# Kernel tuning notes

Hardware: AMD Instinct MI355X
Metric: run time of the kernel (lower is better)

## Reference

```python
import jax, jax.numpy as jnp
import numpy as np
import math

DIM_EMB = 1024
DIM_QK = 1024
DIM_V = 1024
NORM_FACT = 1.0 / math.sqrt(DIM_EMB)

def setup_inputs() -> dict:
    key = jax.random.key(0)
    k0, k1, k2, k3 = jax.random.split(key, 4)
    x = jax.random.normal(k0, (4, 4096, DIM_EMB), dtype=jnp.float32)
    # nn.Linear weights are [out_features, in_features]; y = x @ W.T
    s = 1.0 / math.sqrt(DIM_EMB)
    Wq = jax.random.uniform(k1, (DIM_QK, DIM_EMB), jnp.float32, -s, s)
    Wk = jax.random.uniform(k2, (DIM_QK, DIM_EMB), jnp.float32, -s, s)
    Wv = jax.random.uniform(k3, (DIM_V, DIM_EMB), jnp.float32, -s, s)
    return {"x": x, "Wq": Wq, "Wk": Wk, "Wv": Wv}

def reference(x, Wq, Wk, Wv):
    # q,k,v: [b, n, d]
    q = jnp.einsum('bne,de->bnd', x, Wq)
    k = jnp.einsum('bne,de->bnd', x, Wk)
    v = jnp.einsum('bne,de->bnd', x, Wv)
    logits = jnp.einsum('bnd,bmd->bnm', q, k)  # [b, n, n]
    # Faithful to source: softmax over last dim FIRST, then scale by 1/sqrt(dim_embedding)
    score = jax.nn.softmax(logits, axis=-1) * NORM_FACT
    att = jnp.einsum('bnm,bmv->bnv', score, v)
    return att
```

## Files before the change

kernel.cpp:

```cpp
#include <hip/hip_runtime.h>
#include <hip/hip_bf16.h>

typedef _Float16 f16;
typedef _Float16 f16x4 __attribute__((ext_vector_type(4)));
typedef _Float16 f16x8 __attribute__((ext_vector_type(8)));
typedef float f32x4 __attribute__((ext_vector_type(4)));

__device__ __forceinline__ void gload16(const void* g, void* l) {
    __builtin_amdgcn_global_load_lds(
        (const __attribute__((address_space(1))) void*)g,
        (__attribute__((address_space(3))) void*)l, 16, 0, 0);
}

#define FENCE asm volatile("" ::: "memory")
#define BARRIER do { FENCE; __builtin_amdgcn_s_barrier(); FENCE; } while (0)

#define PHASE_MFMA(QI, QJ)                                                    \
    __builtin_amdgcn_s_setprio(1);                                            \
    _Pragma("unroll")                                                         \
    for (int ks = 0; ks < 2; ++ks)                                            \
      _Pragma("unroll")                                                       \
      for (int i = 0; i < 4; ++i)                                             \
        _Pragma("unroll")                                                     \
        for (int j = 0; j < 2; ++j)                                           \
          acc[(QI)*4 + i][(QJ)*2 + j] = __builtin_amdgcn_mfma_f32_16x16x32_f16( \
              a[i][ks], b[j][ks], acc[(QI)*4 + i][(QJ)*2 + j], 0, 0, 0);      \
    __builtin_amdgcn_s_setprio(0);

#define BT8_BODY(KBASE, NTILES)                                               \
    const int rr8 = lane >> 3;                                                \
    const int cs  = ((lane & 7) ^ rr8) << 3;                                  \
    const int ldsr = wid << 3;                                                \
    auto stageA = [&](int kt, int c, int h) {                                 \
        const size_t g0 = (size_t)(bm + (h << 7) + ldsr + rr8) * lda + (KBASE) + kt + cs; \
        gload16(A + g0,                      &sA[c][((h << 7) + ldsr) << 6]); \
        gload16(A + g0 + ((size_t)lda << 6), &sA[c][((h << 7) + 64 + ldsr) << 6]); \
    };                                                                        \
    auto stageB = [&](int kt, int c, int h) {                                 \
        const size_t g0 = (size_t)(bn + (h << 7) + ldsr + rr8) * ldb + (KBASE) + kt + cs; \
        gload16(B + g0,                      &sB[c][((h << 7) + ldsr) << 6]); \
        gload16(B + g0 + ((size_t)ldb << 6), &sB[c][((h << 7) + 64 + ldsr) << 6]); \
    };                                                                        \
    f32x4 acc[8][4] = {};                                                     \
    f16x8 a[4][2], b[2][2];                                                   \
    auto loadA = [&](int c, int qi) {                                         \
        _Pragma("unroll")                                                     \
        for (int i = 0; i < 4; ++i) {                                         \
            const int ra = wr * 128 + (qi * 4 + i) * 16 + (lane & 15);        \
            const int swz = (ra & 7) << 3;                                    \
            _Pragma("unroll")                                                 \
            for (int ks = 0; ks < 2; ++ks) {                                  \
                const int kk = ks * 32 + (lane >> 4) * 8;                     \
                a[i][ks] = *(const f16x8*)(&sA[c][(ra << 6) + (kk ^ swz)]);   \
            }                                                                 \
        }                                                                     \
    };                                                                        \
    auto loadB = [&](int c, int qj) {                                         \
        _Pragma("unroll")                                                     \
        for (int j = 0; j < 2; ++j) {                                         \
            const int rb = wc * 64 + (qj * 2 + j) * 16 + (lane & 15);         \
            const int swz = (rb & 7) << 3;                                    \
            _Pragma("unroll")                                                 \
            for (int ks = 0; ks < 2; ++ks) {                                  \
                const int kk = ks * 32 + (lane >> 4) * 8;                     \
                b[j][ks] = *(const f16x8*)(&sB[c][(rb << 6) + (kk ^ swz)]);   \
            }                                                                 \
        }                                                                     \
    };                                                                        \
    stageA(0, 0, 0); stageA(0, 0, 1); stageB(0, 0, 0); stageB(0, 0, 1);       \
    for (int g = 0; g < (NTILES); ++g) {                                      \
        const int c = g & 1, cn = c ^ 1;                                      \
        const int kn = (g + 1) << 6;                                          \
        const bool more = (g + 1) < (NTILES);                                 \
              \
        if (more) {                                                           \
            stageA(kn, cn, 0); stageA(kn, cn, 1);                             \
            asm volatile("s_waitcnt vmcnt(4)" ::: "memory");                  \
        } else {                                                              \
            asm volatile("s_waitcnt vmcnt(0)" ::: "memory");                  \
        }                                                                     \
        BARRIER;                                                              \
        loadA(c, 0); loadB(c, 0);                                             \
        BARRIER; PHASE_MFMA(0, 0); BARRIER;                                   \
                                       \
        if (more) { stageB(kn, cn, 0); stageB(kn, cn, 1); }                   \
        loadB(c, 1);                                                          \
        BARRIER; PHASE_MFMA(0, 1); BARRIER;                                   \
                                                                     \
        loadA(c, 1); loadB(c, 0);                                             \
        BARRIER; PHASE_MFMA(1, 0); BARRIER;                                   \
                                                                     \
        loadB(c, 1);                                                          \
        BARRIER; PHASE_MFMA(1, 1); BARRIER;                                   \
    }

template<bool F16OUT>
__global__ __launch_bounds__(512) void gemm_bt8(
    const f16* __restrict__ A, const f16* __restrict__ B, void* __restrict__ Cv,
    int K, int lda, int ldb, int ldc, float scale, int nbn)
{
    __shared__ f16 sA[2][256 * 64];
    __shared__ f16 sB[2][256 * 64];
    const int tid = threadIdx.x, lane = tid & 63, wid = tid >> 6;
    const int wr = wid >> 2, wc = wid & 3;
    const int cpx = gridDim.x >> 3;
    const int wg = (blockIdx.x & 7) * cpx + (blockIdx.x >> 3);
    const int bm = (wg / nbn) << 8, bn = (wg % nbn) << 8;

    BT8_BODY(0, K >> 6)

#pragma unroll
    for (int i = 0; i < 8; ++i)
#pragma unroll
        for (int j = 0; j < 4; ++j)
#pragma unroll
            for (int r = 0; r < 4; ++r) {
                const int row = bm + wr * 128 + i * 16 + ((lane >> 4) << 2) + r;
                const int col = bn + wc * 64 + j * 16 + (lane & 15);
                if constexpr (F16OUT)
                    ((f16*)Cv)[(size_t)row * ldc + col] = (f16)(acc[i][j][r] * scale);
                else
                    ((float*)Cv)[(size_t)row * ldc + col] = acc[i][j][r] * scale;
            }
}

__global__ __launch_bounds__(512) void gemm_qk(
    const f16* __restrict__ A, const f16* __restrict__ B,
    f16* __restrict__ S, int lda, int ldb)
{
    __shared__ f16 sA[2][256 * 64];
    __shared__ f16 sB[2][256 * 64];
    const int tid = threadIdx.x, lane = tid & 63, wid = tid >> 6;
    const int wr = wid >> 2, wc = wid & 3;
    const int cpx = gridDim.x >> 3;
    const int wg = (blockIdx.x & 7) * cpx + (blockIdx.x >> 3);
    const int bm = (wg >> 4) << 8, bn = (wg & 15) << 8;

    BT8_BODY(0, 16)

    {
        f16* Tb = wr ? (f16*)sB : (f16*)sA;
        const int lg = lane >> 4;
#pragma unroll
        for (int i = 0; i < 8; ++i)
#pragma unroll
            for (int j = 0; j < 4; ++j)
#pragma unroll
                for (int r = 0; r < 4; ++r) {
                    const int rloc = i * 16 + lg * 4 + r;
                    const int col  = wc * 64 + j * 16 + (lane & 15);
                    Tb[rloc * 256 + (col ^ (((rloc >> 2) & 7) << 3))] = (f16)acc[i][j][r];
                }
    }
    BARRIER;
#pragma unroll
    for (int u = 0; u < 16; ++u) {
        const int gi = u * 512 + tid;
        const int row = gi >> 5;
        const int c0 = (gi & 31) << 3;
        const f16* Tb = (row & 128) ? (const f16*)sB : (const f16*)sA;
        f16x8 v = *(const f16x8*)(Tb + (row & 127) * 256
                                  + (c0 ^ (((row >> 2) & 7) << 3)));
        *(f16x8*)(S + (size_t)(bm + row) * 4096 + bn + c0) = v;
    }
}

__global__ __launch_bounds__(256) void softmax_f16(f16* S)
{
    const int lane = threadIdx.x & 63, wid = threadIdx.x >> 6;
    const int row = blockIdx.x * 4 + wid;
    f16* src = S + (size_t)row * 4096;
    f16x8 v[8];
#pragma unroll
    for (int u = 0; u < 8; ++u) v[u] = *(const f16x8*)(src + u * 512 + lane * 8);
    float m = -1e30f;
#pragma unroll
    for (int u = 0; u < 8; ++u)
#pragma unroll
        for (int e = 0; e < 8; ++e) m = fmaxf(m, (float)v[u][e]);
#pragma unroll
    for (int msk = 1; msk <= 32; msk <<= 1) m = fmaxf(m, __shfl_xor(m, msk));
    float ev[64];
    float s = 0.f;
#pragma unroll
    for (int u = 0; u < 8; ++u)
#pragma unroll
        for (int e = 0; e < 8; ++e) {
            const float x = __expf((float)v[u][e] - m);
            ev[u * 8 + e] = x; s += x;
        }
#pragma unroll
    for (int msk = 1; msk <= 32; msk <<= 1) s += __shfl_xor(s, msk);
    const float inv = 1.0f / (32.0f * s);
#pragma unroll
    for (int u = 0; u < 8; ++u) {
        f16x8 p;
#pragma unroll
        for (int e = 0; e < 8; ++e) p[e] = (f16)(ev[u * 8 + e] * inv);
        *(f16x8*)(src + u * 512 + lane * 8) = p;
    }
}

__global__ __launch_bounds__(512) void gemm_pv8(
    const f16* __restrict__ A, const f16* __restrict__ B, float* __restrict__ Cout,
    f16* __restrict__ Pp, int lda, int ldb)
{
    __shared__ f16 sA[2][256 * 64];
    __shared__ f16 sB[2][256 * 64];
    const int tid = threadIdx.x, lane = tid & 63, wid = tid >> 6;
    const int wr = wid >> 2, wc = wid & 3;
    const int cpx = gridDim.x >> 3;
    const int wg = (blockIdx.x & 7) * cpx + (blockIdx.x >> 3);
    const int bm = (wg >> 2) << 8, bn = (wg & 3) << 8;
    const int z = blockIdx.y;
    const int kbase = z << 10;

    BT8_BODY(kbase, 16)

#pragma unroll
    for (int i = 0; i < 8; ++i)
#pragma unroll
        for (int j = 0; j < 4; ++j)
#pragma unroll
            for (int r = 0; r < 4; ++r) {
                const int row = bm + wr * 128 + i * 16 + ((lane >> 4) << 2) + r;
                const int col = bn + wc * 64 + j * 16 + (lane & 15);
                const float v = acc[i][j][r];
                if (z == 3)
                    Cout[((size_t)row << 10) + col] = v;
                else
                    Pp[(size_t)z * 4194304 + ((size_t)row << 10) + col] = (f16)v;
            }
}

__global__ __launch_bounds__(256) void reduce_pv(
    float* __restrict__ Cout, const f16* __restrict__ Pp)
{
    const int i = blockIdx.x * 256 + threadIdx.x;
    const int r = i >> 7;
    const int c = (i & 127) << 3;
    const size_t base = ((size_t)r << 10) + c;
    const f16x8 p0 = *(const f16x8*)(Pp + base);
    const f16x8 p1 = *(const f16x8*)(Pp + base + 4194304);
    const f16x8 p2 = *(const f16x8*)(Pp + base + 8388608);
    float* o = Cout + base;
    float4 o0 = *(float4*)o, o1 = *(float4*)(o + 4);
    o0.x += (float)p0[0] + (float)p1[0] + (float)p2[0];
    o0.y += (float)p0[1] + (float)p1[1] + (float)p2[1];
    o0.z += (float)p0[2] + (float)p1[2] + (float)p2[2];
    o0.w += (float)p0[3] + (float)p1[3] + (float)p2[3];
    o1.x += (float)p0[4] + (float)p1[4] + (float)p2[4];
    o1.y += (float)p0[5] + (float)p1[5] + (float)p2[5];
    o1.z += (float)p0[6] + (float)p1[6] + (float)p2[6];
    o1.w += (float)p0[7] + (float)p1[7] + (float)p2[7];
    *(float4*)o = o0;
    *(float4*)(o + 4) = o1;
}

__global__ __launch_bounds__(256) void gemm_vt(
    const f16* __restrict__ A, const f16* __restrict__ B, f16* __restrict__ C,
    int K, int lda, int ldb, int ldc)
{
    __shared__ f16 sA[2][128 * 64];
    __shared__ f16 sB[2][128 * 64];
    const int tid = threadIdx.x, lane = tid & 63, wid = tid >> 6;
    const int wr = wid >> 1, wc = wid & 1;
    const int bm = blockIdx.x * 128, bn = blockIdx.y * 128;

    f32x4 acc[4][4] = {};

    auto stage16 = [&](int kt, int bsel) {
        const int rsub = lane >> 3;
        const int csw = ((lane & 7) ^ rsub) << 3;
#pragma unroll
        for (int i = 0; i < 4; ++i) {
            const int rb = (wid * 4 + i) * 8;
            gload16(A + (size_t)(bm + rb + rsub) * lda + kt + csw, &sA[bsel][rb * 64]);
            gload16(B + (size_t)(bn + rb + rsub) * ldb + kt + csw, &sB[bsel][rb * 64]);
        }
    };

    auto compute = [&](int bsel) {
#pragma unroll
        for (int ks = 0; ks < 2; ++ks) {
            const int kk = ks * 32 + (lane >> 4) * 8;
            f16x8 a[4], b[4];
#pragma unroll
            for (int i = 0; i < 4; ++i) {
                const int ra = wr * 64 + i * 16 + (lane & 15);
                a[i] = *(const f16x8*)(&sA[bsel][(ra << 6) + (kk ^ ((ra & 7) << 3))]);
                const int rb2 = wc * 64 + i * 16 + (lane & 15);
                b[i] = *(const f16x8*)(&sB[bsel][(rb2 << 6) + (kk ^ ((rb2 & 7) << 3))]);
            }
#pragma unroll
            for (int i = 0; i < 4; ++i)
#pragma unroll
                for (int j = 0; j < 4; ++j)
                    acc[i][j] = __builtin_amdgcn_mfma_f32_16x16x32_f16(a[i], b[j], acc[i][j], 0, 0, 0);
        }
    };

    stage16(0, 0);
    asm volatile("s_waitcnt vmcnt(0)" ::: "memory");
    __syncthreads();
    const int NT2 = K >> 6;
    for (int t = 0; t < NT2; ++t) {
        if (t + 1 < NT2) stage16((t + 1) << 6, (t + 1) & 1);
        compute(t & 1);
        asm volatile("s_waitcnt vmcnt(0)" ::: "memory");
        __builtin_amdgcn_s_barrier();
    }
#pragma unroll
    for (int i = 0; i < 4; ++i)
#pragma unroll
        for (int j = 0; j < 4; ++j)
#pragma unroll
            for (int r = 0; r < 4; ++r) {
                const int row = bm + wr * 64 + i * 16 + (lane >> 4) * 4 + r;
                const int col = bn + wc * 64 + j * 16 + (lane & 15);
                C[(size_t)row * ldc + col] = (f16)acc[i][j][r];
            }
}

__global__ __launch_bounds__(256) void cvt3(
    const float* __restrict__ x, const float* __restrict__ wq, const float* __restrict__ wk,
    f16* __restrict__ dx, f16* __restrict__ dwq, f16* __restrict__ dwk)
{
    const int i = blockIdx.x * 256 + threadIdx.x;
    const float* s; f16* d; int off;
    if (i < 2097152)      { s = x;  d = dx;  off = i; }
    else if (i < 2228224) { s = wq; d = dwq; off = i - 2097152; }
    else                  { s = wk; d = dwk; off = i - 2228224; }
    const float4 a = ((const float4*)s)[off * 2];
    const float4 b = ((const float4*)s)[off * 2 + 1];
    f16x8 o = { (f16)a.x, (f16)a.y, (f16)a.z, (f16)a.w,
                (f16)b.x, (f16)b.y, (f16)b.z, (f16)b.w };
    ((f16x8*)d)[off] = o;
}

__global__ __launch_bounds__(256) void cvt_batch(
    const float* __restrict__ xb, const float* __restrict__ wv,
    f16* __restrict__ dxb, f16* __restrict__ dwv)
{
    const int i = blockIdx.x * 256 + threadIdx.x;
    const float* s; f16* d; int off;
    if (i < 524288) { s = xb; d = dxb; off = i; }
    else            { s = wv; d = dwv; off = i - 524288; }
    const float4 a = ((const float4*)s)[off * 2];
    const float4 b = ((const float4*)s)[off * 2 + 1];
    f16x8 o = { (f16)a.x, (f16)a.y, (f16)a.z, (f16)a.w,
                (f16)b.x, (f16)b.y, (f16)b.z, (f16)b.w };
    ((f16x8*)d)[off] = o;
}

extern "C" void kernel_launch(void* const* d_in, const int* in_sizes, int n_in,
                              void* d_out, int out_size, void* d_ws, size_t ws_size,
                              hipStream_t stream) {
    const float* x  = (const float*)d_in[0];
    const float* Wq = (const float*)d_in[1];
    const float* Wk = (const float*)d_in[2];
    const float* Wv = (const float*)d_in[3];
    float* out = (float*)d_out;

    f16*   qk  = (f16*)d_out;
    f16*   xh  = (f16*)d_ws;
    f16*   wqh = (f16*)((char*)d_ws + (32LL << 20));
    f16*   wkh = wqh + 1024LL * 1024;

    f16*   S   = (f16*)d_ws;
    f16*   Pp  = (f16*)((char*)d_ws + (32LL << 20));
    f16*   vTw = (f16*)((char*)d_ws + (56LL << 20));

    cvt3<<<9216, 256, 0, stream>>>(x, Wq, Wk, xh, wqh, wkh);

    gemm_bt8<true><<<256, 512, 0, stream>>>(xh, wqh, qk,        1024, 1024, 1024, 2048, 1.f, 4);
    gemm_bt8<true><<<256, 512, 0, stream>>>(xh, wkh, qk + 1024, 1024, 1024, 1024, 2048, 1.f, 4);

    for (int b = 0; b < 4; ++b) {
        const size_t tb = (size_t)b * 4096;
        f16* xhb = (f16*)(out + tb * 1024);
        f16* wvh = xhb + 4096LL * 1024;
        gemm_qk<<<256, 512, 0, stream>>>(
            qk + tb * 2048, qk + tb * 2048 + 1024, S, 2048, 2048);
        softmax_f16<<<1024, 256, 0, stream>>>(S);
        cvt_batch<<<2560, 256, 0, stream>>>(x + tb * 1024, Wv, xhb, wvh);
        gemm_vt<<<dim3(8, 32), 256, 0, stream>>>(wvh, xhb, vTw, 1024, 1024, 1024, 4096);
        gemm_pv8<<<dim3(64, 4), 512, 0, stream>>>(S, vTw, out + tb * 1024, Pp, 4096, 4096);
        reduce_pv<<<2048, 256, 0, stream>>>(out + tb * 1024, Pp);
    }
}
```

Before: 673.5 us.

## Unroll GEMM k-loop by two and spread async LDS stages across MFMA phases

Restructures the shared GEMM main loop into a two-tile unrolled schedule. Global-to-LDS stage loads are interleaved at finer granularity between the MFMA phases, and the B register fragments are kept for both column halves so they no longer need reloading. The number of barriers per tile drops from eight to four. The aim is more overlap of memory traffic with MFMA work and fewer LDS reads. The cost is more registers, and the loop now assumes an even tile count.

```diff
diff --git a/kernel.cpp b/kernel.cpp
--- a/kernel.cpp
+++ b/kernel.cpp
@@ -24,7 +24,7 @@
         _Pragma("unroll")                                                     \
         for (int j = 0; j < 2; ++j)                                           \
           acc[(QI)*4 + i][(QJ)*2 + j] = __builtin_amdgcn_mfma_f32_16x16x32_f16( \
-              a[i][ks], b[j][ks], acc[(QI)*4 + i][(QJ)*2 + j], 0, 0, 0);      \
+              a[i][ks], b[(QJ)*2 + j][ks], acc[(QI)*4 + i][(QJ)*2 + j], 0, 0, 0); \
     __builtin_amdgcn_s_setprio(0);
 
 #define BT8_BODY(KBASE, NTILES)                                               \
@@ -42,7 +42,7 @@
         gload16(B + g0 + ((size_t)ldb << 6), &sB[c][((h << 7) + 64 + ldsr) << 6]); \
     };                                                                        \
     f32x4 acc[8][4] = {};                                                     \
-    f16x8 a[4][2], b[2][2];                                                   \
+    f16x8 a[4][2], b[4][2];                                                   \
     auto loadA = [&](int c, int qi) {                                         \
         _Pragma("unroll")                                                     \
         for (int i = 0; i < 4; ++i) {                                         \
@@ -50,7 +50,7 @@
             const int swz = (ra & 7) << 3;                                    \
             _Pragma("unroll")                                                 \
             for (int ks = 0; ks < 2; ++ks) {                                  \
-                const int kk = ks * 32 + (lane >> 4) * 8;                     \
+                const int kk = ks * 32 + ((lane >> 4) << 3);                  \
                 a[i][ks] = *(const f16x8*)(&sA[c][(ra << 6) + (kk ^ swz)]);   \
             }                                                                 \
         }                                                                     \
@@ -62,36 +62,63 @@
             const int swz = (rb & 7) << 3;                                    \
             _Pragma("unroll")                                                 \
             for (int ks = 0; ks < 2; ++ks) {                                  \
-                const int kk = ks * 32 + (lane >> 4) * 8;                     \
-                b[j][ks] = *(const f16x8*)(&sB[c][(rb << 6) + (kk ^ swz)]);   \
+                const int kk = ks * 32 + ((lane >> 4) << 3);                  \
+                b[qj * 2 + j][ks] = *(const f16x8*)(&sB[c][(rb << 6) + (kk ^ swz)]); \
             }                                                                 \
         }                                                                     \
     };                                                                        \
+            \
     stageA(0, 0, 0); stageA(0, 0, 1); stageB(0, 0, 0); stageB(0, 0, 1);       \
-    for (int g = 0; g < (NTILES); ++g) {                                      \
-        const int c = g & 1, cn = c ^ 1;                                      \
-        const int kn = (g + 1) << 6;                                          \
-        const bool more = (g + 1) < (NTILES);                                 \
-              \
+    stageA(64, 1, 0);                                                         \
+    for (int g2 = 0; g2 < (NTILES); g2 += 2) {                                \
+        const bool more = (g2 + 2) < (NTILES);                                \
+        const int kO  = (g2 + 1) << 6;                                        \
+        const int kE2 = (g2 + 2) << 6;                                        \
+        const int kO2 = (g2 + 3) << 6;                                        \
+           \
+        stageA(kO, 1, 1); stageB(kO, 1, 0);                                   \
+        asm volatile("s_waitcnt vmcnt(6)" ::: "memory");                      \
+        BARRIER;                                                              \
+        loadA(0, 0); loadB(0, 0);                                             \
+        PHASE_MFMA(0, 0);                                                     \
+        BARRIER;                                                              \
+                                           \
+        stageB(kO, 1, 1);                                                     \
+        loadB(0, 1);                                                          \
+        PHASE_MFMA(0, 1);                                                     \
+        BARRIER;                                                              \
+                                                        \
+        loadA(0, 1);                                                          \
+        PHASE_MFMA(1, 0);                                                     \
+        BARRIER;                                                              \
+                                                       \
+        if (more) stageA(kE2, 0, 0);                                          \
+        PHASE_MFMA(1, 1);                                                     \
+        BARRIER;                                                              \
+         \
         if (more) {                                                           \
-            stageA(kn, cn, 0); stageA(kn, cn, 1);                             \
-            asm volatile("s_waitcnt vmcnt(4)" ::: "memory");                  \
+            stageA(kE2, 0, 1); stageB(kE2, 0, 0);                             \
+            asm volatile("s_waitcnt vmcnt(6)" ::: "memory");                  \
         } else {                                                              \
             asm volatile("s_waitcnt vmcnt(0)" ::: "memory");                  \
         }                                                                     \
         BARRIER;                                                              \
-        loadA(c, 0); loadB(c, 0);                                             \
-        BARRIER; PHASE_MFMA(0, 0); BARRIER;                                   \
-                                       \
-        if (more) { stageB(kn, cn, 0); stageB(kn, cn, 1); }                   \
-        loadB(c, 1);                                                          \
-        BARRIER; PHASE_MFMA(0, 1); BARRIER;                                   \
-                                                                     \
-        loadA(c, 1); loadB(c, 0);                                             \
-        BARRIER; PHASE_MFMA(1, 0); BARRIER;                                   \
-                                                                     \
-        loadB(c, 1);                                                          \
-        BARRIER; PHASE_MFMA(1, 1); BARRIER;                                   \
+        loadA(1, 0); loadB(1, 0);                                             \
+        PHASE_MFMA(0, 0);                                                     \
+        BARRIER;                                                              \
+                                          \
+        if (more) stageB(kE2, 0, 1);                                          \
+        loadB(1, 1);                                                          \
+        PHASE_MFMA(0, 1);                                                     \
+        BARRIER;                                                              \
+                                                        \
+        loadA(1, 1);                                                          \
+        PHASE_MFMA(1, 0);                                                     \
+        BARRIER;                                                              \
+                                                       \
+        if (more) stageA(kO2, 1, 0);                                          \
+        PHASE_MFMA(1, 1);                                                     \
+        BARRIER;                                                              \
     }
 
 template<bool F16OUT>
```

After: 569.1 us. -15.5%, faster.
